# Kernel tuning notes

Hardware: AMD Instinct MI355X
Metric: run time of the kernel (lower is better)

The kernel has to match this reference:

```python
import jax, jax.numpy as jnp
import numpy as np

B, H, D = 16, 32, 128          # batch, heads, head_dim
NB, BS, MB = 1024, 16, 128     # num cache blocks, block_size, max blocks per seq
HIDDEN = H * D
EPS = 1e-6


def setup_inputs() -> dict:
    key = jax.random.key(0)
    ks = jax.random.split(key, 5)
    return {
        "hidden_states": jax.random.normal(ks[0], (B, HIDDEN), dtype=jnp.float32),
        "key_cache": jax.random.normal(ks[1], (NB, BS, H, D), dtype=jnp.float32),
        "value_cache": jax.random.normal(ks[2], (NB, BS, H, D), dtype=jnp.float32),
        "block_tables": jax.random.randint(ks[3], (B, MB), 0, NB, dtype=jnp.int32),
        "context_lens": jax.random.randint(ks[4], (B,), 1, MB * BS + 1, dtype=jnp.int32),
        "rms_weight": jnp.ones((HIDDEN,), dtype=jnp.float32),
    }


def reference(hidden_states, key_cache, value_cache, block_tables, context_lens, rms_weight):
    bsz = hidden_states.shape[0]
    nb, bs, h, d = key_cache.shape
    scale = 1.0 / np.sqrt(d).astype(np.float32)

    residual = hidden_states
    # RMSNorm
    x = hidden_states
    norm = x * jax.lax.rsqrt(jnp.mean(x * x, axis=-1, keepdims=True) + EPS) * rms_weight
    q = norm.reshape(bsz, h, d)  # [B, H, D] single decode token per sequence

    # Paged KV gather: block_tables [B, MB] indexes into cache blocks
    keys = key_cache[block_tables].reshape(bsz, -1, h, d)    # [B, S, H, D], S = MB*BS
    vals = value_cache[block_tables].reshape(bsz, -1, h, d)  # [B, S, H, D]
    s = keys.shape[1]

    scores = jnp.einsum('bhd,bshd->bhs', q, keys) * scale    # [B, H, S]
    valid = jnp.arange(s, dtype=jnp.int32)[None, :] < context_lens[:, None]  # [B, S]
    scores = jnp.where(valid[:, None, :], scores, -jnp.inf)
    probs = jax.nn.softmax(scores, axis=-1)
    attn = jnp.einsum('bhs,bshd->bhd', probs, vals).reshape(bsz, h * d)

    return residual + attn
```

## Files before the change

kernel.cpp:

```cpp
#include <hip/hip_runtime.h>
#include <math.h>

#define BATCH 16
#define NHEAD 32
#define HDIM 128
#define HIDDEN 4096
#define BS 16
#define MB 128
#define EPS 1e-6f
#define NWORK 8

__global__ __launch_bounds__(256) void rmsnorm_kernel(const float* __restrict__ x,
                                                      const float* __restrict__ w,
                                                      float* __restrict__ q) {
    int b = blockIdx.x;
    int tid = threadIdx.x;
    const float4* xr = (const float4*)(x + (size_t)b * HIDDEN);
    float4 xs[4];
    float ss = 0.f;
#pragma unroll
    for (int i = 0; i < 4; i++) {
        float4 v = xr[tid + i * 256];
        xs[i] = v;
        ss += v.x * v.x + v.y * v.y + v.z * v.z + v.w * v.w;
    }
#pragma unroll
    for (int m = 32; m >= 1; m >>= 1) ss += __shfl_xor(ss, m, 64);
    __shared__ float red[4];
    int wave = tid >> 6;
    if ((tid & 63) == 0) red[wave] = ss;
    __syncthreads();
    float tot = red[0] + red[1] + red[2] + red[3];
    float rstd = rsqrtf(tot * (1.0f / HIDDEN) + EPS);

    const float4* wr = (const float4*)w;
    float4* qr = (float4*)(q + (size_t)b * HIDDEN);
#pragma unroll
    for (int i = 0; i < 4; i++) {
        float4 v = xs[i];
        float4 ww = wr[tid + i * 256];
        float4 o;
        o.x = v.x * rstd * ww.x;
        o.y = v.y * rstd * ww.y;
        o.z = v.z * rstd * ww.z;
        o.w = v.w * rstd * ww.w;
        qr[tid + i * 256] = o;
    }
}

__global__ __launch_bounds__(256) void attn_kernel(const float* __restrict__ q,
                                                   const float* __restrict__ kc,
                                                   const float* __restrict__ vc,
                                                   const int* __restrict__ bt,
                                                   const int* __restrict__ cl,
                                                   const float* __restrict__ resid,
                                                   float* __restrict__ out) {
    const int h = blockIdx.x;
    const int b = blockIdx.y;
    const int tid = threadIdx.x;
    const int w = tid >> 5;
    const int lane = tid & 31;

    __shared__ int s_bt[MB];
    __shared__ float s_m[NWORK];
    __shared__ float s_l[NWORK];
    __shared__ float s_acc[NWORK][HDIM];

    if (tid < MB) s_bt[tid] = bt[b * MB + tid];
    const int L = cl[b];
    float4 q4 = *(const float4*)(q + (size_t)b * HIDDEN + h * HDIM + 4 * lane);
    __syncthreads();

    const float scale = 0.08838834764831845f;
    float m = -INFINITY;
    float l = 0.f;
    float4 acc = make_float4(0.f, 0.f, 0.f, 0.f);

    for (int s = w; s < L; s += NWORK) {
        int blk = s_bt[s >> 4];
        size_t off = ((((size_t)blk * BS + (s & 15)) * NHEAD + h) * HDIM) + 4 * lane;
        float4 k4 = *(const float4*)(kc + off);
        float4 v4 = *(const float4*)(vc + off);
        float dot = k4.x * q4.x + k4.y * q4.y + k4.z * q4.z + k4.w * q4.w;
#pragma unroll
        for (int msk = 16; msk >= 1; msk >>= 1) dot += __shfl_xor(dot, msk, 64);
        float score = dot * scale;
        float mn = fmaxf(m, score);
        float alpha = __expf(m - mn);
        float p = __expf(score - mn);
        l = l * alpha + p;
        acc.x = acc.x * alpha + p * v4.x;
        acc.y = acc.y * alpha + p * v4.y;
        acc.z = acc.z * alpha + p * v4.z;
        acc.w = acc.w * alpha + p * v4.w;
        m = mn;
    }

    *((float4*)&s_acc[w][4 * lane]) = acc;
    if (lane == 0) {
        s_m[w] = m;
        s_l[w] = l;
    }
    __syncthreads();

    if (tid < HDIM) {
        float M = -INFINITY;
#pragma unroll
        for (int i = 0; i < NWORK; i++) M = fmaxf(M, s_m[i]);
        float Ls = 0.f, A = 0.f;
#pragma unroll
        for (int i = 0; i < NWORK; i++) {
            float sc = __expf(s_m[i] - M);
            Ls += s_l[i] * sc;
            A += s_acc[i][tid] * sc;
        }
        size_t oi = (size_t)b * HIDDEN + h * HDIM + tid;
        out[oi] = resid[oi] + A / Ls;
    }
}

extern "C" void kernel_launch(void* const* d_in, const int* in_sizes, int n_in,
                              void* d_out, int out_size, void* d_ws, size_t ws_size,
                              hipStream_t stream) {
    const float* hs = (const float*)d_in[0];
    const float* kc = (const float*)d_in[1];
    const float* vc = (const float*)d_in[2];
    const int* bt = (const int*)d_in[3];
    const int* cl = (const int*)d_in[4];
    const float* rw = (const float*)d_in[5];
    float* out = (float*)d_out;
    float* q = (float*)d_ws;

    rmsnorm_kernel<<<BATCH, 256, 0, stream>>>(hs, rw, q);
    attn_kernel<<<dim3(NHEAD, BATCH), 256, 0, stream>>>(q, kc, vc, bt, cl, hs, out);
}
```

Baseline: 560.0 us.

## Split attention over sequence chunks with a separate combine kernel

```diff
diff --git a/kernel.cpp b/kernel.cpp
--- a/kernel.cpp
+++ b/kernel.cpp
@@ -9,6 +9,12 @@
 #define MB 128
 #define EPS 1e-6f
 #define NWORK 8
+#define SPLIT 8
+
+#define Q_FLOATS (BATCH * HIDDEN)
+#define M_OFF Q_FLOATS
+#define L_OFF (M_OFF + BATCH * NHEAD * SPLIT)
+#define A_OFF (L_OFF + BATCH * NHEAD * SPLIT)
 
 __global__ __launch_bounds__(256) void rmsnorm_kernel(const float* __restrict__ x,
                                                       const float* __restrict__ w,
@@ -48,15 +54,17 @@
     }
 }
 
-__global__ __launch_bounds__(256) void attn_kernel(const float* __restrict__ q,
-                                                   const float* __restrict__ kc,
-                                                   const float* __restrict__ vc,
-                                                   const int* __restrict__ bt,
-                                                   const int* __restrict__ cl,
-                                                   const float* __restrict__ resid,
-                                                   float* __restrict__ out) {
+__global__ __launch_bounds__(256) void attn_partial_kernel(const float* __restrict__ ws,
+                                                           const float* __restrict__ kc,
+                                                           const float* __restrict__ vc,
+                                                           const int* __restrict__ bt,
+                                                           const int* __restrict__ cl,
+                                                           float* __restrict__ pm,
+                                                           float* __restrict__ pl,
+                                                           float* __restrict__ pacc) {
     const int h = blockIdx.x;
     const int b = blockIdx.y;
+    const int si = blockIdx.z;
     const int tid = threadIdx.x;
     const int w = tid >> 5;
     const int lane = tid & 31;
@@ -66,9 +74,13 @@
     __shared__ float s_l[NWORK];
     __shared__ float s_acc[NWORK][HDIM];
 
+    const int L = cl[b];
+    const int chunk = (L + SPLIT - 1) / SPLIT;
+    const int s0 = si * chunk;
+    const int s1 = min(s0 + chunk, L);
+
     if (tid < MB) s_bt[tid] = bt[b * MB + tid];
-    const int L = cl[b];
-    float4 q4 = *(const float4*)(q + (size_t)b * HIDDEN + h * HDIM + 4 * lane);
+    float4 q4 = *(const float4*)(ws + (size_t)b * HIDDEN + h * HDIM + 4 * lane);
     __syncthreads();
 
     const float scale = 0.08838834764831845f;
@@ -76,9 +88,36 @@
     float l = 0.f;
     float4 acc = make_float4(0.f, 0.f, 0.f, 0.f);
 
-    for (int s = w; s < L; s += NWORK) {
-        int blk = s_bt[s >> 4];
-        size_t off = ((((size_t)blk * BS + (s & 15)) * NHEAD + h) * HDIM) + 4 * lane;
+    int s = s0 + w;
+    for (; s + NWORK < s1; s += 2 * NWORK) {
+        int sB = s + NWORK;
+        size_t offA = ((((size_t)s_bt[s >> 4] * BS + (s & 15)) * NHEAD + h) * HDIM) + 4 * lane;
+        size_t offB = ((((size_t)s_bt[sB >> 4] * BS + (sB & 15)) * NHEAD + h) * HDIM) + 4 * lane;
+        float4 kA = *(const float4*)(kc + offA);
+        float4 kB = *(const float4*)(kc + offB);
+        float4 vA = *(const float4*)(vc + offA);
+        float4 vB = *(const float4*)(vc + offB);
+        float dA = kA.x * q4.x + kA.y * q4.y + kA.z * q4.z + kA.w * q4.w;
+        float dB = kB.x * q4.x + kB.y * q4.y + kB.z * q4.z + kB.w * q4.w;
+#pragma unroll
+        for (int msk = 16; msk >= 1; msk >>= 1) {
+            dA += __shfl_xor(dA, msk, 64);
+            dB += __shfl_xor(dB, msk, 64);
+        }
+        float scA = dA * scale, scB = dB * scale;
+        float mn = fmaxf(m, fmaxf(scA, scB));
+        float alpha = __expf(m - mn);
+        float p0 = __expf(scA - mn);
+        float p1 = __expf(scB - mn);
+        l = l * alpha + p0 + p1;
+        acc.x = acc.x * alpha + p0 * vA.x + p1 * vB.x;
+        acc.y = acc.y * alpha + p0 * vA.y + p1 * vB.y;
+        acc.z = acc.z * alpha + p0 * vA.z + p1 * vB.z;
+        acc.w = acc.w * alpha + p0 * vA.w + p1 * vB.w;
+        m = mn;
+    }
+    for (; s < s1; s += NWORK) {
+        size_t off = ((((size_t)s_bt[s >> 4] * BS + (s & 15)) * NHEAD + h) * HDIM) + 4 * lane;
         float4 k4 = *(const float4*)(kc + off);
         float4 v4 = *(const float4*)(vc + off);
         float dot = k4.x * q4.x + k4.y * q4.y + k4.z * q4.z + k4.w * q4.w;
@@ -107,16 +146,46 @@
         float M = -INFINITY;
 #pragma unroll
         for (int i = 0; i < NWORK; i++) M = fmaxf(M, s_m[i]);
-        float Ls = 0.f, A = 0.f;
-#pragma unroll
-        for (int i = 0; i < NWORK; i++) {
-            float sc = __expf(s_m[i] - M);
-            Ls += s_l[i] * sc;
-            A += s_acc[i][tid] * sc;
+        size_t pbase = ((size_t)(b * NHEAD + h) * SPLIT + si);
+        if (M == -INFINITY) {
+            if (tid == 0) { pm[pbase] = -INFINITY; pl[pbase] = 0.f; }
+            pacc[pbase * HDIM + tid] = 0.f;
+        } else {
+            float Ls = 0.f, A = 0.f;
+#pragma unroll
+            for (int i = 0; i < NWORK; i++) {
+                float sc = __expf(s_m[i] - M);
+                Ls += s_l[i] * sc;
+                A += s_acc[i][tid] * sc;
+            }
+            if (tid == 0) { pm[pbase] = M; pl[pbase] = Ls; }
+            pacc[pbase * HDIM + tid] = A;
         }
-        size_t oi = (size_t)b * HIDDEN + h * HDIM + tid;
-        out[oi] = resid[oi] + A / Ls;
-    }
+    }
+}
+
+__global__ __launch_bounds__(128) void attn_combine_kernel(const float* __restrict__ pm,
+                                                           const float* __restrict__ pl,
+                                                           const float* __restrict__ pacc,
+                                                           const float* __restrict__ resid,
+                                                           float* __restrict__ out) {
+    const int h = blockIdx.x;
+    const int b = blockIdx.y;
+    const int tid = threadIdx.x;
+    size_t pbase = (size_t)(b * NHEAD + h) * SPLIT;
+
+    float M = -INFINITY;
+#pragma unroll
+    for (int i = 0; i < SPLIT; i++) M = fmaxf(M, pm[pbase + i]);
+    float Ls = 0.f, A = 0.f;
+#pragma unroll
+    for (int i = 0; i < SPLIT; i++) {
+        float sc = __expf(pm[pbase + i] - M);
+        Ls += pl[pbase + i] * sc;
+        A += pacc[(pbase + i) * HDIM + tid] * sc;
+    }
+    size_t oi = (size_t)b * HIDDEN + h * HDIM + tid;
+    out[oi] = resid[oi] + A / Ls;
 }
 
 extern "C" void kernel_launch(void* const* d_in, const int* in_sizes, int n_in,
@@ -129,8 +198,14 @@
     const int* cl = (const int*)d_in[4];
     const float* rw = (const float*)d_in[5];
     float* out = (float*)d_out;
-    float* q = (float*)d_ws;
+    float* ws = (float*)d_ws;
+    float* q = ws;
+    float* pm = ws + M_OFF;
+    float* pl = ws + L_OFF;
+    float* pacc = ws + A_OFF;
 
     rmsnorm_kernel<<<BATCH, 256, 0, stream>>>(hs, rw, q);
-    attn_kernel<<<dim3(NHEAD, BATCH), 256, 0, stream>>>(q, kc, vc, bt, cl, hs, out);
-}
+    attn_partial_kernel<<<dim3(NHEAD, BATCH, SPLIT), 256, 0, stream>>>(q, kc, vc, bt, cl,
+                                                                       pm, pl, pacc);
+    attn_combine_kernel<<<dim3(NHEAD, BATCH), 128, 0, stream>>>(pm, pl, pacc, hs, out);
+}
```

New measurement: 496.1 us. 11.4% less time.
